# Kernel optimization log

Hardware: AMD Instinct MI355X
Metric: run time of the kernel (lower is better)

The kernel has to match this reference:

```python
import jax, jax.numpy as jnp
import numpy as np

N = 50000
E = 600000


def gcn_conv(x, W, b, src, dst, n):
    # PyG GCNConv: h = x @ W; add self-loops; symmetric normalization; aggregate; + bias
    h = x @ W  # [N, out]
    deg = jnp.zeros((n,), h.dtype).at[dst].add(1.0) + 1.0  # self-loop included
    dinv = jax.lax.rsqrt(deg)  # deg >= 1, always finite
    coef = dinv[src] * dinv[dst]  # [E]
    msg = h[src] * coef[:, None]  # [E, out]  (the memory-bound gather)
    agg = jax.ops.segment_sum(msg, dst, num_segments=n)
    agg = agg + h * (dinv * dinv)[:, None]  # self-loop contribution
    return agg + b


def setup_inputs() -> dict:
    key = jax.random.key(0)
    ks = jax.random.split(key, 8)
    x = jax.random.normal(ks[0], (N, 128), dtype=jnp.float32)
    edge_index = jax.random.randint(ks[1], (2, E), 0, N, dtype=jnp.int64 if jax.config.jax_enable_x64 else jnp.int32)
    def glorot(k, fan_in, fan_out):
        s = jnp.sqrt(6.0 / (fan_in + fan_out))
        return jax.random.uniform(k, (fan_in, fan_out), jnp.float32, -s, s)
    W1 = glorot(ks[2], 128, 128)
    b1 = jnp.zeros((128,), jnp.float32)
    W2 = glorot(ks[3], 128, 64)
    b2 = jnp.zeros((64,), jnp.float32)
    W3 = glorot(ks[4], 64, 16)
    b3 = jnp.zeros((16,), jnp.float32)
    return {"x": x, "edge_index": edge_index, "W1": W1, "b1": b1, "W2": W2, "b2": b2, "W3": W3, "b3": b3}


def reference(x, edge_index, W1, b1, W2, b2, W3, b3):
    src, dst = edge_index[0], edge_index[1]
    n = x.shape[0]
    h = jax.nn.relu(gcn_conv(x, W1, b1, src, dst, n))
    h = jax.nn.relu(gcn_conv(h, W2, b2, src, dst, n))
    h = gcn_conv(h, W3, b3, src, dst, n)
    return h
```

## Files before the change

kernel.cpp:

```cpp
#include <hip/hip_runtime.h>
#include <hip/hip_fp16.h>
#include <type_traits>


typedef _Float16 f16x8 __attribute__((ext_vector_type(8)));
typedef float f32x4 __attribute__((ext_vector_type(4)));

#define CSR_CAP 64

__device__ inline float2 h2f(unsigned int u) {
  __half2 h = __builtin_bit_cast(__half2, u);
  return __half22float2(h);
}

__device__ inline void fma8h(float4& a0, float4& a1, const uint4& g, float w) {
  float2 f0 = h2f(g.x), f1 = h2f(g.y), f2 = h2f(g.z), f3 = h2f(g.w);
  a0.x = fmaf(f0.x, w, a0.x);
  a0.y = fmaf(f0.y, w, a0.y);
  a0.z = fmaf(f1.x, w, a0.z);
  a0.w = fmaf(f1.y, w, a0.w);
  a1.x = fmaf(f2.x, w, a1.x);
  a1.y = fmaf(f2.y, w, a1.y);
  a1.z = fmaf(f3.x, w, a1.z);
  a1.w = fmaf(f3.y, w, a1.w);
}

__device__ inline unsigned int pack2h(float x, float y) {
  __half2 h = __floats2half2_rn(x, y);
  return __builtin_bit_cast(unsigned int, h);
}

__device__ inline uint2 pack4h(const float4& v) {
  uint2 r;
  r.x = pack2h(v.x, v.y);
  r.y = pack2h(v.z, v.w);
  return r;
}


__global__ void scatter_kernel(const int* __restrict__ src, const int* __restrict__ dst,
                               const int* __restrict__ cnt, int* __restrict__ cur,
                               int2* __restrict__ csr, int E) {
  int e = blockIdx.x * blockDim.x + threadIdx.x;
  if (e < E) {
    int s = src[e];
    int d = dst[e];
    float w = rsqrtf((float)cnt[s] + 1.0f) * rsqrtf((float)cnt[d] + 1.0f);
    int pos = atomicAdd(&cur[d], 1);
    if (pos >= CSR_CAP) pos = CSR_CAP - 1;
    int2 pk;
    pk.x = s;
    pk.y = __float_as_int(w);
    csr[(size_t)d * CSR_CAP + pos] = pk;
  }
}

template <int K, int F, typename TIN>
__global__ __launch_bounds__(256) void gemm_mfma(const TIN* __restrict__ A,
                                                 const float* __restrict__ W,
                                                 __half* __restrict__ C16, int n,
                                                 int nwaves, int ngemm,
                                                 const int* __restrict__ dst,
                                                 int* __restrict__ cnt, int E) {
  constexpr int KP = K + 8;
  constexpr int KS = K / 32;
  constexpr int NT = F / 16;

  if (blockIdx.x >= ngemm) {
    int base = (blockIdx.x - ngemm) * 256 + threadIdx.x;
    int stride = (gridDim.x - ngemm) * 256;
    for (int e = base; e < E; e += stride) atomicAdd(&cnt[dst[e]], 1);
    return;
  }

  __shared__ __half Ws[F * KP];

  int t = threadIdx.x;
  for (int i = t; i < K * F; i += 256) {
    int kk = i / F, nn = i % F;
    Ws[nn * KP + kk] = __float2half(W[i]);
  }
  __syncthreads();

  int wave = blockIdx.x * 4 + (t >> 6);
  if (wave >= nwaves) return;
  int lane = t & 63;
  int m = lane & 15;
  int quad = lane >> 4;

  int arow = wave * 16 + m;
  if (arow >= n) arow = n - 1;

  f16x8 af[KS];
  if constexpr (std::is_same_v<TIN, float>) {
#pragma unroll
    for (int ks = 0; ks < KS; ++ks) {
      const float* p = A + (size_t)arow * K + ks * 32 + quad * 8;
      float4 lo = *(const float4*)p;
      float4 hi = *(const float4*)(p + 4);
      f16x8 a;
      a[0] = (_Float16)lo.x; a[1] = (_Float16)lo.y;
      a[2] = (_Float16)lo.z; a[3] = (_Float16)lo.w;
      a[4] = (_Float16)hi.x; a[5] = (_Float16)hi.y;
      a[6] = (_Float16)hi.z; a[7] = (_Float16)hi.w;
      af[ks] = a;
    }
  } else {
#pragma unroll
    for (int ks = 0; ks < KS; ++ks)
      af[ks] = *(const f16x8*)(const void*)&A[(size_t)arow * K + ks * 32 + quad * 8];
  }

  f32x4 acc[NT];
#pragma unroll
  for (int nt = 0; nt < NT; ++nt) acc[nt] = (f32x4){0.f, 0.f, 0.f, 0.f};
#pragma unroll
  for (int nt = 0; nt < NT; ++nt)
#pragma unroll
    for (int ks = 0; ks < KS; ++ks) {
      f16x8 b = *(const f16x8*)(const void*)&Ws[(nt * 16 + m) * KP + ks * 32 + quad * 8];
      acc[nt] = __builtin_amdgcn_mfma_f32_16x16x32_f16(af[ks], b, acc[nt], 0, 0, 0);
    }

  int rbase = wave * 16 + quad * 4;
#pragma unroll
  for (int nt = 0; nt < NT; ++nt)
#pragma unroll
    for (int r = 0; r < 4; ++r) {
      int rr = rbase + r;
      if (rr < n) C16[(size_t)rr * F + nt * 16 + m] = __float2half(acc[nt][r]);
    }
}

template <int K, int F, int CPL, int EU>
__global__ __launch_bounds__(512) void aggmm(
    const __half* __restrict__ hprev, const float* __restrict__ W,
    const float* __restrict__ bias, const int* __restrict__ cnt,
    const int2* __restrict__ csr, __half* __restrict__ C16, int n) {
  constexpr int KP = K + 8;
  constexpr int KS = K / 32;
  constexpr int NT = F / 16;
  constexpr int TPN = 8;
  constexpr int RS = K / 8;
  static_assert(TPN * CPL == RS, "chunk coverage");

  __shared__ __half Ws[F * KP];
  __shared__ __half As[64 * KP];

  int t = threadIdx.x;
  for (int i = t; i < K * F; i += 512) {
    int kk = i / F, nn = i % F;
    Ws[nn * KP + kk] = __float2half(W[i]);
  }

  int wid = t >> 6;
  int lane = t & 63;
  int nb = blockIdx.x * 64;

  {
    int sub = lane / TPN;
    int fl = lane % TPN;
    int nib = wid * 8 + sub;
    int node = nb + nib;
    int nd = node < n ? node : n - 1;
    const uint4* h4 = (const uint4*)hprev;
    int c0 = cnt[nd];
    float di = rsqrtf((float)c0 + 1.0f);
    float sc = di * di;
    float4 acc[CPL][2];
#pragma unroll
    for (int c = 0; c < CPL; ++c) {
      acc[c][0] = make_float4(0.f, 0.f, 0.f, 0.f);
      acc[c][1] = make_float4(0.f, 0.f, 0.f, 0.f);
    }
#pragma unroll
    for (int c = 0; c < CPL; ++c) {
      uint4 sv = h4[(size_t)nd * RS + fl + c * TPN];
      fma8h(acc[c][0], acc[c][1], sv, sc);
    }
    int j = nd * CSR_CAP;
    int e = j + c0;
    for (; j + EU <= e; j += EU) {
      int2 p[EU];
#pragma unroll
      for (int u = 0; u < EU; ++u) p[u] = csr[j + u];
      uint4 g[EU][CPL];
#pragma unroll
      for (int u = 0; u < EU; ++u)
#pragma unroll
        for (int c = 0; c < CPL; ++c) g[u][c] = h4[(size_t)p[u].x * RS + fl + c * TPN];
#pragma unroll
      for (int u = 0; u < EU; ++u)
#pragma unroll
        for (int c = 0; c < CPL; ++c)
          fma8h(acc[c][0], acc[c][1], g[u][c], __int_as_float(p[u].y));
    }
    for (; j < e; ++j) {
      int2 p = csr[j];
#pragma unroll
      for (int c = 0; c < CPL; ++c) {
        uint4 g = h4[(size_t)p.x * RS + fl + c * TPN];
        fma8h(acc[c][0], acc[c][1], g, __int_as_float(p.y));
      }
    }
#pragma unroll
    for (int c = 0; c < CPL; ++c) {
      int ch = fl + c * TPN;
      float4 b0 = *(const float4*)&bias[ch * 8];
      float4 b1 = *(const float4*)&bias[ch * 8 + 4];
      float4 r0 = make_float4(fmaxf(acc[c][0].x + b0.x, 0.f), fmaxf(acc[c][0].y + b0.y, 0.f),
                              fmaxf(acc[c][0].z + b0.z, 0.f), fmaxf(acc[c][0].w + b0.w, 0.f));
      float4 r1 = make_float4(fmaxf(acc[c][1].x + b1.x, 0.f), fmaxf(acc[c][1].y + b1.y, 0.f),
                              fmaxf(acc[c][1].z + b1.z, 0.f), fmaxf(acc[c][1].w + b1.w, 0.f));
      uint2 lo = pack4h(r0), hi = pack4h(r1);
      uint4 pk;
      pk.x = lo.x; pk.y = lo.y; pk.z = hi.x; pk.w = hi.y;
      *(uint4*)&As[(size_t)nib * KP + ch * 8] = pk;
    }
  }

  __syncthreads();

  if (wid < 4) {
    int m = lane & 15;
    int quad = lane >> 4;
    const __half* At = &As[(size_t)wid * 16 * KP];
    f16x8 af[KS];
#pragma unroll
    for (int ks = 0; ks < KS; ++ks)
      af[ks] = *(const f16x8*)(const void*)&At[m * KP + ks * 32 + quad * 8];

    f32x4 acc2[NT];
#pragma unroll
    for (int nt = 0; nt < NT; ++nt) acc2[nt] = (f32x4){0.f, 0.f, 0.f, 0.f};
#pragma unroll
    for (int nt = 0; nt < NT; ++nt)
#pragma unroll
      for (int ks = 0; ks < KS; ++ks) {
        f16x8 bfr = *(const f16x8*)(const void*)&Ws[(nt * 16 + m) * KP + ks * 32 + quad * 8];
        acc2[nt] = __builtin_amdgcn_mfma_f32_16x16x32_f16(af[ks], bfr, acc2[nt], 0, 0, 0);
      }

    int rbase = nb + wid * 16 + quad * 4;
#pragma unroll
    for (int nt = 0; nt < NT; ++nt)
#pragma unroll
      for (int r = 0; r < 4; ++r) {
        int rr = rbase + r;
        if (rr < n) C16[(size_t)rr * F + nt * 16 + m] = __float2half(acc2[nt][r]);
      }
  }
}

__global__ __launch_bounds__(256) void agg_final(
    const __half* __restrict__ h16, const int* __restrict__ cnt,
    const int2* __restrict__ csr, const float* __restrict__ bias,
    float* __restrict__ out, int n) {
  int node = blockIdx.x * 64 + threadIdx.x / 4;
  int q = threadIdx.x & 3;
  int half = q >> 1;
  int fl = q & 1;
  bool valid = node < n;
  int nd = valid ? node : n - 1;

  const uint4* h4 = (const uint4*)h16;
  int c0 = cnt[nd];
  float di = rsqrtf((float)c0 + 1.0f);
  float4 a0 = make_float4(0.f, 0.f, 0.f, 0.f);
  float4 a1 = make_float4(0.f, 0.f, 0.f, 0.f);
  if (half == 0) {
    uint4 sv = h4[(size_t)nd * 2 + fl];
    fma8h(a0, a1, sv, di * di);
  }
  int s = nd * CSR_CAP;
  int e = s + c0;
  int j = s + half;
  for (; j + 2 < e; j += 4) {
    int2 p0 = csr[j];
    int2 p1 = csr[j + 2];
    uint4 g0 = h4[(size_t)p0.x * 2 + fl];
    uint4 g1 = h4[(size_t)p1.x * 2 + fl];
    fma8h(a0, a1, g0, __int_as_float(p0.y));
    fma8h(a0, a1, g1, __int_as_float(p1.y));
  }
  for (; j < e; j += 2) {
    int2 p = csr[j];
    uint4 g = h4[(size_t)p.x * 2 + fl];
    fma8h(a0, a1, g, __int_as_float(p.y));
  }

  a0.x += __shfl_xor(a0.x, 2);
  a0.y += __shfl_xor(a0.y, 2);
  a0.z += __shfl_xor(a0.z, 2);
  a0.w += __shfl_xor(a0.w, 2);
  a1.x += __shfl_xor(a1.x, 2);
  a1.y += __shfl_xor(a1.y, 2);
  a1.z += __shfl_xor(a1.z, 2);
  a1.w += __shfl_xor(a1.w, 2);

  if (valid && half == 0) {
    float4 b0 = *(const float4*)&bias[fl * 8];
    float4 b1 = *(const float4*)&bias[fl * 8 + 4];
    float4 r0 = make_float4(a0.x + b0.x, a0.y + b0.y, a0.z + b0.z, a0.w + b0.w);
    float4 r1 = make_float4(a1.x + b1.x, a1.y + b1.y, a1.z + b1.z, a1.w + b1.w);
    float* op = &out[(size_t)node * 16 + fl * 8];
    *(float4*)op = r0;
    *(float4*)(op + 4) = r1;
  }
}


extern "C" void kernel_launch(void* const* d_in, const int* in_sizes, int n_in,
                              void* d_out, int out_size, void* d_ws, size_t ws_size,
                              hipStream_t stream) {
  const float* x = (const float*)d_in[0];
  const int* edge = (const int*)d_in[1];
  const float* W1 = (const float*)d_in[2];
  const float* b1 = (const float*)d_in[3];
  const float* W2 = (const float*)d_in[4];
  const float* b2 = (const float*)d_in[5];
  const float* W3 = (const float*)d_in[6];
  const float* b3 = (const float*)d_in[7];

  const int N = in_sizes[0] / 128;
  const int E = in_sizes[1] / 2;
  const int* src = edge;
  const int* dstp = edge + E;
  float* out = (float*)d_out;

  size_t off = 0;
  auto take = [&](size_t bytes) -> void* {
    void* r = (char*)d_ws + off;
    off += (bytes + 255) & ~(size_t)255;
    return r;
  };
  int* cnt = (int*)take((size_t)N * 4);
  int* cur = (int*)take((size_t)N * 4);
  int2* csr = (int2*)take((size_t)N * CSR_CAP * 8);
  __half* t1 = (__half*)take((size_t)N * 128 * 2);
  __half* t2 = (__half*)take((size_t)N * 64 * 2);
  __half* t3 = (__half*)take((size_t)N * 16 * 2);

  hipMemsetAsync(d_ws, 0, 2 * (((size_t)N * 4 + 255) & ~(size_t)255), stream);

  const int TB = 256;
  int eg = (E + TB - 1) / TB;
  int nwaves = (N + 15) / 16;
  int gblk = (nwaves + 3) / 4;
  int fblk = (N + 63) / 64;
  int cblk = 512;

  gemm_mfma<128, 128, float><<<gblk + cblk, 256, 0, stream>>>(x, W1, t1, N, nwaves, gblk,
                                                              dstp, cnt, E);
  scatter_kernel<<<eg, TB, 0, stream>>>(src, dstp, cnt, cur, csr, E);

  aggmm<128, 64, 2, 4><<<fblk, 512, 0, stream>>>(t1, W2, b1, cnt, csr, t2, N);
  aggmm<64, 16, 1, 4><<<fblk, 512, 0, stream>>>(t2, W3, b2, cnt, csr, t3, N);
  agg_final<<<fblk, 256, 0, stream>>>(t3, cnt, csr, b3, out, N);
}
```

Before: 197.0 us.

## Fuse CSR build into GEMM launch and compute edge weights on the fly

Removes the separate degree-count pass and scatter kernel. Edges are bucketed directly into the padded CSR inside the first GEMM launch, and the per-slot atomic counter doubles as the degree. CSR entries shrink from (src, weight) pairs to plain src indices. Aggregation kernels now recompute the normalization per edge from the degree array and software-prefetch the next batch of indices, trading extra small gathers and rsqrt work for one fewer kernel launch, one fewer atomic pass and half the CSR traffic.

```diff
diff --git a/kernel.cpp b/kernel.cpp
--- a/kernel.cpp
+++ b/kernel.cpp
@@ -37,39 +37,27 @@
   return r;
 }
 
-
-__global__ void scatter_kernel(const int* __restrict__ src, const int* __restrict__ dst,
-                               const int* __restrict__ cnt, int* __restrict__ cur,
-                               int2* __restrict__ csr, int E) {
-  int e = blockIdx.x * blockDim.x + threadIdx.x;
-  if (e < E) {
-    int s = src[e];
-    int d = dst[e];
-    float w = rsqrtf((float)cnt[s] + 1.0f) * rsqrtf((float)cnt[d] + 1.0f);
-    int pos = atomicAdd(&cur[d], 1);
-    if (pos >= CSR_CAP) pos = CSR_CAP - 1;
-    int2 pk;
-    pk.x = s;
-    pk.y = __float_as_int(w);
-    csr[(size_t)d * CSR_CAP + pos] = pk;
-  }
-}
-
 template <int K, int F, typename TIN>
 __global__ __launch_bounds__(256) void gemm_mfma(const TIN* __restrict__ A,
                                                  const float* __restrict__ W,
                                                  __half* __restrict__ C16, int n,
                                                  int nwaves, int ngemm,
+                                                 const int* __restrict__ src,
                                                  const int* __restrict__ dst,
-                                                 int* __restrict__ cnt, int E) {
+                                                 int* __restrict__ cur,
+                                                 int* __restrict__ csr, int E) {
   constexpr int KP = K + 8;
   constexpr int KS = K / 32;
   constexpr int NT = F / 16;
 
   if (blockIdx.x >= ngemm) {
-    int base = (blockIdx.x - ngemm) * 256 + threadIdx.x;
-    int stride = (gridDim.x - ngemm) * 256;
-    for (int e = base; e < E; e += stride) atomicAdd(&cnt[dst[e]], 1);
+    int e = (blockIdx.x - ngemm) * 256 + threadIdx.x;
+    if (e < E) {
+      int d = dst[e];
+      int pos = atomicAdd(&cur[d], 1);
+      if (pos >= CSR_CAP) pos = CSR_CAP - 1;
+      csr[(size_t)d * CSR_CAP + pos] = src[e];
+    }
     return;
   }
 
@@ -136,7 +124,7 @@
 __global__ __launch_bounds__(512) void aggmm(
     const __half* __restrict__ hprev, const float* __restrict__ W,
     const float* __restrict__ bias, const int* __restrict__ cnt,
-    const int2* __restrict__ csr, __half* __restrict__ C16, int n) {
+    const int* __restrict__ csr, __half* __restrict__ C16, int n) {
   constexpr int KP = K + 8;
   constexpr int KS = K / 32;
   constexpr int NT = F / 16;
@@ -167,6 +155,7 @@
     int c0 = cnt[nd];
     float di = rsqrtf((float)c0 + 1.0f);
     float sc = di * di;
+    int cc = c0 < CSR_CAP ? c0 : CSR_CAP;
     float4 acc[CPL][2];
 #pragma unroll
     for (int c = 0; c < CPL; ++c) {
@@ -179,28 +168,41 @@
       fma8h(acc[c][0], acc[c][1], sv, sc);
     }
     int j = nd * CSR_CAP;
-    int e = j + c0;
-    for (; j + EU <= e; j += EU) {
-      int2 p[EU];
-#pragma unroll
-      for (int u = 0; u < EU; ++u) p[u] = csr[j + u];
+    int e = j + cc;
+    int p[EU];
+#pragma unroll
+    for (int u = 0; u < EU; ++u) p[u] = csr[j + u];
+    for (; j + EU <= e;) {
       uint4 g[EU][CPL];
 #pragma unroll
       for (int u = 0; u < EU; ++u)
 #pragma unroll
-        for (int c = 0; c < CPL; ++c) g[u][c] = h4[(size_t)p[u].x * RS + fl + c * TPN];
-#pragma unroll
-      for (int u = 0; u < EU; ++u)
-#pragma unroll
-        for (int c = 0; c < CPL; ++c)
-          fma8h(acc[c][0], acc[c][1], g[u][c], __int_as_float(p[u].y));
-    }
-    for (; j < e; ++j) {
-      int2 p = csr[j];
-#pragma unroll
-      for (int c = 0; c < CPL; ++c) {
-        uint4 g = h4[(size_t)p.x * RS + fl + c * TPN];
-        fma8h(acc[c][0], acc[c][1], g, __int_as_float(p.y));
+        for (int c = 0; c < CPL; ++c) g[u][c] = h4[(size_t)p[u] * RS + fl + c * TPN];
+      int cs[EU];
+#pragma unroll
+      for (int u = 0; u < EU; ++u) cs[u] = cnt[p[u]];
+      j += EU;
+      int pn[EU];
+#pragma unroll
+      for (int u = 0; u < EU; ++u) pn[u] = csr[j + u];
+#pragma unroll
+      for (int u = 0; u < EU; ++u) {
+        float w = rsqrtf((float)cs[u] + 1.0f) * di;
+#pragma unroll
+        for (int c = 0; c < CPL; ++c) fma8h(acc[c][0], acc[c][1], g[u][c], w);
+      }
+#pragma unroll
+      for (int u = 0; u < EU; ++u) p[u] = pn[u];
+    }
+#pragma unroll
+    for (int u = 0; u < EU; ++u) {
+      if (j + u < e) {
+        float w = rsqrtf((float)cnt[p[u]] + 1.0f) * di;
+#pragma unroll
+        for (int c = 0; c < CPL; ++c) {
+          uint4 g = h4[(size_t)p[u] * RS + fl + c * TPN];
+          fma8h(acc[c][0], acc[c][1], g, w);
+        }
       }
     }
 #pragma unroll
@@ -254,7 +256,7 @@
 
 __global__ __launch_bounds__(256) void agg_final(
     const __half* __restrict__ h16, const int* __restrict__ cnt,
-    const int2* __restrict__ csr, const float* __restrict__ bias,
+    const int* __restrict__ csr, const float* __restrict__ bias,
     float* __restrict__ out, int n) {
   int node = blockIdx.x * 64 + threadIdx.x / 4;
   int q = threadIdx.x & 3;
@@ -266,6 +268,7 @@
   const uint4* h4 = (const uint4*)h16;
   int c0 = cnt[nd];
   float di = rsqrtf((float)c0 + 1.0f);
+  int cc = c0 < CSR_CAP ? c0 : CSR_CAP;
   float4 a0 = make_float4(0.f, 0.f, 0.f, 0.f);
   float4 a1 = make_float4(0.f, 0.f, 0.f, 0.f);
   if (half == 0) {
@@ -273,20 +276,22 @@
     fma8h(a0, a1, sv, di * di);
   }
   int s = nd * CSR_CAP;
-  int e = s + c0;
+  int e = s + cc;
   int j = s + half;
   for (; j + 2 < e; j += 4) {
-    int2 p0 = csr[j];
-    int2 p1 = csr[j + 2];
-    uint4 g0 = h4[(size_t)p0.x * 2 + fl];
-    uint4 g1 = h4[(size_t)p1.x * 2 + fl];
-    fma8h(a0, a1, g0, __int_as_float(p0.y));
-    fma8h(a0, a1, g1, __int_as_float(p1.y));
+    int p0 = csr[j];
+    int p1 = csr[j + 2];
+    int ca = cnt[p0];
+    int cb = cnt[p1];
+    uint4 g0 = h4[(size_t)p0 * 2 + fl];
+    uint4 g1 = h4[(size_t)p1 * 2 + fl];
+    fma8h(a0, a1, g0, rsqrtf((float)ca + 1.0f) * di);
+    fma8h(a0, a1, g1, rsqrtf((float)cb + 1.0f) * di);
   }
   for (; j < e; j += 2) {
-    int2 p = csr[j];
-    uint4 g = h4[(size_t)p.x * 2 + fl];
-    fma8h(a0, a1, g, __int_as_float(p.y));
+    int p = csr[j];
+    uint4 g = h4[(size_t)p * 2 + fl];
+    fma8h(a0, a1, g, rsqrtf((float)cnt[p] + 1.0f) * di);
   }
 
   a0.x += __shfl_xor(a0.x, 2);
@@ -334,27 +339,23 @@
     off += (bytes + 255) & ~(size_t)255;
     return r;
   };
-  int* cnt = (int*)take((size_t)N * 4);
   int* cur = (int*)take((size_t)N * 4);
-  int2* csr = (int2*)take((size_t)N * CSR_CAP * 8);
+  int* csr = (int*)take((size_t)N * CSR_CAP * 4 + 256);
   __half* t1 = (__half*)take((size_t)N * 128 * 2);
   __half* t2 = (__half*)take((size_t)N * 64 * 2);
   __half* t3 = (__half*)take((size_t)N * 16 * 2);
 
-  hipMemsetAsync(d_ws, 0, 2 * (((size_t)N * 4 + 255) & ~(size_t)255), stream);
-
-  const int TB = 256;
-  int eg = (E + TB - 1) / TB;
+  hipMemsetAsync(d_ws, 0, ((size_t)N * 4 + 255) & ~(size_t)255, stream);
+
   int nwaves = (N + 15) / 16;
   int gblk = (nwaves + 3) / 4;
   int fblk = (N + 63) / 64;
-  int cblk = 512;
-
-  gemm_mfma<128, 128, float><<<gblk + cblk, 256, 0, stream>>>(x, W1, t1, N, nwaves, gblk,
-                                                              dstp, cnt, E);
-  scatter_kernel<<<eg, TB, 0, stream>>>(src, dstp, cnt, cur, csr, E);
-
-  aggmm<128, 64, 2, 4><<<fblk, 512, 0, stream>>>(t1, W2, b1, cnt, csr, t2, N);
-  aggmm<64, 16, 1, 4><<<fblk, 512, 0, stream>>>(t2, W3, b2, cnt, csr, t3, N);
-  agg_final<<<fblk, 256, 0, stream>>>(t3, cnt, csr, b3, out, N);
-}
+  int eg = (E + 255) / 256;
+
+  gemm_mfma<128, 128, float><<<gblk + eg, 256, 0, stream>>>(x, W1, t1, N, nwaves, gblk,
+                                                            src, dstp, cur, csr, E);
+
+  aggmm<128, 64, 2, 4><<<fblk, 512, 0, stream>>>(t1, W2, b1, cur, csr, t2, N);
+  aggmm<64, 16, 1, 4><<<fblk, 512, 0, stream>>>(t2, W3, b2, cur, csr, t3, N);
+  agg_final<<<fblk, 256, 0, stream>>>(t3, cur, csr, b3, out, N);
+}
```

Measured after the change: 181.1 us. -8.1%, faster.
